# Optimization experiments

Measured on AMD Instinct MI355X. Metric: run time of the kernel, lower is better.

The kernel has to match this reference:

```python
import jax, jax.numpy as jnp
import numpy as np

D_MODEL = 1024
NUM_HEADS = 16
HEAD_DIM = D_MODEL // NUM_HEADS


def setup_inputs() -> dict:
    key = jax.random.key(0)
    k_x, k_wqkv, k_bqkv, k_wo, k_bo = jax.random.split(key, 5)
    s = 1.0 / np.sqrt(D_MODEL)
    return {
        "x": jax.random.normal(k_x, (4, 2048, D_MODEL), dtype=jnp.float32),
        "W_qkv": jax.random.uniform(k_wqkv, (D_MODEL, 3 * D_MODEL), jnp.float32, -s, s),
        "b_qkv": jax.random.uniform(k_bqkv, (3 * D_MODEL,), jnp.float32, -s, s),
        "W_out": jax.random.uniform(k_wo, (D_MODEL, D_MODEL), jnp.float32, -s, s),
        "b_out": jax.random.uniform(k_bo, (D_MODEL,), jnp.float32, -s, s),
    }


def reference(x, W_qkv, b_qkv, W_out, b_out):
    B, N, C = x.shape
    # fused QKV projection -> [B, N, 3, H, Dh]
    qkv = (x @ W_qkv + b_qkv).reshape(B, N, 3, NUM_HEADS, HEAD_DIM)
    q = jnp.transpose(qkv[:, :, 0], (0, 2, 1, 3))  # [B, H, N, Dh]
    k = jnp.transpose(qkv[:, :, 1], (0, 2, 1, 3))
    v = jnp.transpose(qkv[:, :, 2], (0, 2, 1, 3))
    scale = 1.0 / jnp.sqrt(jnp.asarray(HEAD_DIM, dtype=x.dtype))
    attn = jnp.einsum('bhqd,bhkd->bhqk', q, k) * scale  # [B, H, N, N]
    attn = jax.nn.softmax(attn, axis=-1)
    # dropout is identity in eval mode
    out = jnp.einsum('bhqk,bhkd->bhqd', attn, v)  # [B, H, N, Dh]
    out = jnp.transpose(out, (0, 2, 1, 3)).reshape(B, N, C)
    return out @ W_out + b_out
```

## Files before the change

kernel.cpp:

```cpp
#include <hip/hip_runtime.h>


typedef __bf16 bf16x8 __attribute__((ext_vector_type(8)));
typedef float f32x4 __attribute__((ext_vector_type(4)));

#define DEV __device__ __forceinline__

DEV unsigned short f2b(float x) {
  unsigned int u = __float_as_uint(x);
  u += 0x7fffu + ((u >> 16) & 1u);
  return (unsigned short)(u >> 16);
}

DEV unsigned int pk_bf16(float a, float b) {
  unsigned int ua = __float_as_uint(a) + 0x8000u;
  unsigned int ub = __float_as_uint(b) + 0x8000u;
  return __builtin_amdgcn_perm(ub, ua, 0x07060302u);
}

#if __has_builtin(__builtin_amdgcn_exp2f)
DEV float exp2_fast(float x) { return __builtin_amdgcn_exp2f(x); }
#else
DEV float exp2_fast(float x) { return exp2f(x); }
#endif

DEV void g2l16(const void* g, void* l) {
  __builtin_amdgcn_global_load_lds(
      (const __attribute__((address_space(1))) unsigned int*)(unsigned long long)g,
      (__attribute__((address_space(3))) unsigned int*)(unsigned int)(unsigned long long)l,
      16, 0, 0);
}

__global__ void cvt_x_kernel(const float* __restrict__ x,
                             unsigned short* __restrict__ xb) {
  int i = blockIdx.x * blockDim.x + threadIdx.x;
  float4 v = ((const float4*)x)[i];
  ushort4 o;
  o.x = f2b(v.x); o.y = f2b(v.y); o.z = f2b(v.z); o.w = f2b(v.w);
  ((ushort4*)xb)[i] = o;
}

__global__ void cvt_wt_kernel(const float* __restrict__ W,
                              unsigned short* __restrict__ Wt,
                              int K, int N) {
  __shared__ float tile[32][33];
  int n0 = blockIdx.x * 32, k0 = blockIdx.y * 32;
  int tx = threadIdx.x, ty = threadIdx.y;
#pragma unroll
  for (int i = 0; i < 32; i += 8)
    tile[ty + i][tx] = W[(size_t)(k0 + ty + i) * N + n0 + tx];
  __syncthreads();
#pragma unroll
  for (int i = 0; i < 32; i += 8)
    Wt[(size_t)(n0 + ty + i) * K + k0 + tx] = f2b(tile[tx][ty + i]);
}

#define QSCALE 0.18033688011112042f

template <int MODE>
__global__ __launch_bounds__(256, 2)
void gemm_bt_kernel(const unsigned short* __restrict__ A,
                    const unsigned short* __restrict__ Bt,
                    const float* __restrict__ bias,
                    unsigned short* __restrict__ qkout,
                    unsigned short* __restrict__ vtout,
                    float* __restrict__ fout) {
  constexpr int K = 1024;
  __shared__ unsigned short As[128 * 32];
  __shared__ unsigned short Bs[128 * 32];

  const int tid = threadIdx.x;
  const int lane = tid & 63;
  const int w = tid >> 6;
  const int wm = w & 1, wn = w >> 1;
  const int l15 = lane & 15, quad = lane >> 4;
  const int m0 = blockIdx.y * 128;
  const int n0 = blockIdx.x * 128;

  const unsigned short* Ag = A + (size_t)m0 * K;
  const unsigned short* Bg = Bt + (size_t)n0 * K;

  const int c0 = tid, c1 = tid + 256;
  const size_t ga0 = (size_t)(c0 >> 2) * K + (size_t)(c0 & 3) * 8;
  const size_t ga1 = (size_t)(c1 >> 2) * K + (size_t)(c1 & 3) * 8;
  unsigned short* la0 = &As[c0 * 8];
  unsigned short* la1 = &As[c1 * 8];
  unsigned short* lb0 = &Bs[c0 * 8];
  unsigned short* lb1 = &Bs[c1 * 8];

  f32x4 acc[4][4] = {};

  for (int kt = 0; kt < K; kt += 32) {
    g2l16(Ag + ga0 + kt, la0);
    g2l16(Ag + ga1 + kt, la1);
    g2l16(Bg + ga0 + kt, lb0);
    g2l16(Bg + ga1 + kt, lb1);
    __syncthreads();
    bf16x8 af[4], bfr[4];
#pragma unroll
    for (int i = 0; i < 4; ++i) {
      af[i]  = *(const bf16x8*)&As[(wm * 64 + i * 16 + l15) * 32 + quad * 8];
      bfr[i] = *(const bf16x8*)&Bs[(wn * 64 + i * 16 + l15) * 32 + quad * 8];
    }
#pragma unroll
    for (int mi = 0; mi < 4; ++mi)
#pragma unroll
      for (int ni = 0; ni < 4; ++ni)
        acc[mi][ni] = __builtin_amdgcn_mfma_f32_16x16x32_bf16(
            af[mi], bfr[ni], acc[mi][ni], 0, 0, 0);
    __syncthreads();
  }

  float bv[4];
#pragma unroll
  for (int ni = 0; ni < 4; ++ni)
    bv[ni] = bias[n0 + wn * 64 + ni * 16 + l15];

  if (MODE == 0) {
    const int sel = n0 >> 10;
    if (sel < 2) {
      const float scale = (sel == 0) ? QSCALE : 1.0f;
      const int csub = (n0 & 1023) + wn * 64;
#pragma unroll
      for (int mi = 0; mi < 4; ++mi) {
        int rb = m0 + wm * 64 + mi * 16 + quad * 4;
#pragma unroll
        for (int ni = 0; ni < 4; ++ni) {
          int c = csub + ni * 16 + l15;
#pragma unroll
          for (int r = 0; r < 4; ++r)
            qkout[(size_t)(rb + r) * 2048 + sel * 1024 + c] =
                f2b((acc[mi][ni][r] + bv[ni]) * scale);
        }
      }
    } else {
#pragma unroll
      for (int mi = 0; mi < 4; ++mi) {
        int rb = m0 + wm * 64 + mi * 16 + quad * 4;
        int bb = rb >> 11, n = rb & 2047;
#pragma unroll
        for (int ni = 0; ni < 4; ++ni) {
          int c = (n0 & 1023) + wn * 64 + ni * 16 + l15;
          int h = c >> 6, d = c & 63;
          ushort4 pk;
          pk.x = f2b(acc[mi][ni][0] + bv[ni]);
          pk.y = f2b(acc[mi][ni][1] + bv[ni]);
          pk.z = f2b(acc[mi][ni][2] + bv[ni]);
          pk.w = f2b(acc[mi][ni][3] + bv[ni]);
          *(ushort4*)&vtout[(((size_t)bb * 16 + h) * 64 + d) * 2048 + n] = pk;
        }
      }
    }
  } else {
#pragma unroll
    for (int mi = 0; mi < 4; ++mi) {
      int rb = m0 + wm * 64 + mi * 16 + quad * 4;
#pragma unroll
      for (int ni = 0; ni < 4; ++ni) {
        int c = n0 + wn * 64 + ni * 16 + l15;
#pragma unroll
        for (int r = 0; r < 4; ++r)
          fout[(size_t)(rb + r) * 1024 + c] = acc[mi][ni][r] + bv[ni];
      }
    }
  }
}

__global__ __launch_bounds__(256, 2)
void attn_kernel(const unsigned short* __restrict__ qk,
                 const unsigned short* __restrict__ vtg,
                 unsigned short* __restrict__ oat) {
  __shared__ unsigned short kt[64 * 72];
  __shared__ unsigned short vt[64 * 72];
  __shared__ unsigned short pt[256 * 72];

  const int tid = threadIdx.x;
  const int lane = tid & 63;
  const int w = tid >> 6;
  const int l15 = lane & 15, quad = lane >> 4;

  const int head = blockIdx.x * 8 + (blockIdx.y >> 3);
  const int qb = blockIdx.y & 7;
  const int b = head >> 4, h = head & 15;
  const int q0 = qb * 256;
  const size_t tokbase = (size_t)b * 2048;

  bf16x8 qf[4][2];
#pragma unroll
  for (int ni = 0; ni < 4; ++ni)
#pragma unroll
    for (int kc = 0; kc < 2; ++kc) {
      int q = q0 + w * 64 + ni * 16 + l15;
      qf[ni][kc] = *(const bf16x8*)(qk + (tokbase + q) * 2048 + h * 64 +
                                    kc * 32 + quad * 8);
    }

  f32x4 oacc[4][4] = {};
  float lsum[4] = {0.f, 0.f, 0.f, 0.f};

  const unsigned short* vhead = vtg + (size_t)head * 64 * 2048;
  const int srow = tid >> 3, spart = tid & 7;
  const int qrow = w * 64 + l15;

  uint4 kreg[2], vreg[2];
#pragma unroll
  for (int it = 0; it < 2; ++it) {
    int row = it * 32 + srow;
    kreg[it] = *(const uint4*)(qk + (tokbase + row) * 2048 + 1024 + h * 64 + spart * 8);
    vreg[it] = *(const uint4*)(vhead + (size_t)row * 2048 + spart * 8);
  }

  for (int kb = 0; kb < 2048; kb += 64) {
    __syncthreads();
#pragma unroll
    for (int it = 0; it < 2; ++it) {
      int row = it * 32 + srow;
      *(uint4*)&kt[row * 72 + spart * 8] = kreg[it];
      *(uint4*)&vt[row * 72 + spart * 8] = vreg[it];
    }
    __syncthreads();

    if (kb + 64 < 2048) {
#pragma unroll
      for (int it = 0; it < 2; ++it) {
        int row = it * 32 + srow;
        kreg[it] = *(const uint4*)(qk + (tokbase + kb + 64 + row) * 2048 + 1024 + h * 64 + spart * 8);
        vreg[it] = *(const uint4*)(vhead + (size_t)row * 2048 + kb + 64 + spart * 8);
      }
    }

    bf16x8 kf[4][2];
#pragma unroll
    for (int mi = 0; mi < 4; ++mi)
#pragma unroll
      for (int kc = 0; kc < 2; ++kc)
        kf[mi][kc] = *(const bf16x8*)&kt[(mi * 16 + l15) * 72 + kc * 32 + quad * 8];

#pragma unroll
    for (int nh = 0; nh < 2; ++nh) {
      f32x4 st[4][2];
#pragma unroll
      for (int mi = 0; mi < 4; ++mi)
#pragma unroll
        for (int nj = 0; nj < 2; ++nj) {
          f32x4 a = {0.f, 0.f, 0.f, 0.f};
          a = __builtin_amdgcn_mfma_f32_16x16x32_bf16(kf[mi][0], qf[nh * 2 + nj][0], a, 0, 0, 0);
          a = __builtin_amdgcn_mfma_f32_16x16x32_bf16(kf[mi][1], qf[nh * 2 + nj][1], a, 0, 0, 0);
          st[mi][nj] = a;
        }
#pragma unroll
      for (int nj = 0; nj < 2; ++nj) {
        int ni = nh * 2 + nj;
        float rs = 0.f;
#pragma unroll
        for (int mi = 0; mi < 4; ++mi) {
          float p0 = exp2_fast(st[mi][nj][0]);
          float p1 = exp2_fast(st[mi][nj][1]);
          float p2 = exp2_fast(st[mi][nj][2]);
          float p3 = exp2_fast(st[mi][nj][3]);
          rs += (p0 + p1) + (p2 + p3);
          uint2 pw;
          pw.x = pk_bf16(p0, p1);
          pw.y = pk_bf16(p2, p3);
          *(uint2*)&pt[(qrow + ni * 16) * 72 + mi * 16 + quad * 4] = pw;
        }
        lsum[ni] += rs;
      }
    }

    bf16x8 pf[4][2];
#pragma unroll
    for (int ni = 0; ni < 4; ++ni)
#pragma unroll
      for (int kc = 0; kc < 2; ++kc)
        pf[ni][kc] = *(const bf16x8*)&pt[(qrow + ni * 16) * 72 + kc * 32 + quad * 8];
#pragma unroll
    for (int df = 0; df < 4; ++df) {
#pragma unroll
      for (int kc = 0; kc < 2; ++kc) {
        bf16x8 vf = *(const bf16x8*)&vt[(df * 16 + l15) * 72 + kc * 32 + quad * 8];
#pragma unroll
        for (int ni = 0; ni < 4; ++ni)
          oacc[df][ni] = __builtin_amdgcn_mfma_f32_16x16x32_bf16(
              vf, pf[ni][kc], oacc[df][ni], 0, 0, 0);
      }
    }
  }

#pragma unroll
  for (int ni = 0; ni < 4; ++ni) {
    float s = lsum[ni];
    s += __shfl_xor(s, 16, 64);
    s += __shfl_xor(s, 32, 64);
    float inv = __builtin_amdgcn_rcpf(s);
    int q = q0 + w * 64 + ni * 16 + l15;
#pragma unroll
    for (int df = 0; df < 4; ++df) {
      uint2 pw;
      pw.x = pk_bf16(oacc[df][ni][0] * inv, oacc[df][ni][1] * inv);
      pw.y = pk_bf16(oacc[df][ni][2] * inv, oacc[df][ni][3] * inv);
      *(uint2*)&oat[(tokbase + q) * 1024 + h * 64 + df * 16 + quad * 4] = pw;
    }
  }
}

extern "C" void kernel_launch(void* const* d_in, const int* in_sizes, int n_in,
                              void* d_out, int out_size, void* d_ws, size_t ws_size,
                              hipStream_t stream) {
  const float* x    = (const float*)d_in[0];
  const float* Wqkv = (const float*)d_in[1];
  const float* bqkv = (const float*)d_in[2];
  const float* Wout = (const float*)d_in[3];
  const float* bout = (const float*)d_in[4];
  float* out = (float*)d_out;

  char* ws = (char*)d_ws;
  unsigned short* xb  = (unsigned short*)(ws + (size_t)0);
  unsigned short* wqt = (unsigned short*)(ws + ((size_t)16 << 20));
  unsigned short* wot = (unsigned short*)(ws + ((size_t)22 << 20));
  unsigned short* qkb = (unsigned short*)(ws + ((size_t)24 << 20));
  unsigned short* vtb = (unsigned short*)(ws + ((size_t)56 << 20));
  unsigned short* oat = (unsigned short*)(ws + ((size_t)72 << 20));

  cvt_x_kernel<<<8192, 256, 0, stream>>>(x, xb);
  cvt_wt_kernel<<<dim3(96, 32), dim3(32, 8), 0, stream>>>(Wqkv, wqt, 1024, 3072);
  cvt_wt_kernel<<<dim3(32, 32), dim3(32, 8), 0, stream>>>(Wout, wot, 1024, 1024);

  gemm_bt_kernel<0><<<dim3(24, 64), 256, 0, stream>>>(
      xb, wqt, bqkv, qkb, vtb, nullptr);

  attn_kernel<<<dim3(8, 64), 256, 0, stream>>>(qkb, vtb, oat);

  gemm_bt_kernel<1><<<dim3(8, 64), 256, 0, stream>>>(
      oat, wot, bout, nullptr, nullptr, out);
}
```

Measured before the change: 312.2 us.

## Pre-swizzle K and V into MFMA fragment layout and load directly to registers

The QKV projection epilogue now writes K and V in a per-head, per-64-key-tile fragment order that matches the MFMA operand layout, and Q goes to its own contiguous buffer. The attention kernel drops its shared-memory staging of K/V tiles and both block barriers per iteration. Each wave instead loads its fragments straight from global memory with coalesced 16-byte loads, double-buffered in registers. The cost is that every wave loads the full K/V tiles redundantly (four times per block, relying on cache), register pressure goes up, and the GEMM epilogue scatter for K is less coalesced.

```diff
diff --git a/kernel.cpp b/kernel.cpp
--- a/kernel.cpp
+++ b/kernel.cpp
@@ -62,8 +62,9 @@
 void gemm_bt_kernel(const unsigned short* __restrict__ A,
                     const unsigned short* __restrict__ Bt,
                     const float* __restrict__ bias,
-                    unsigned short* __restrict__ qkout,
-                    unsigned short* __restrict__ vtout,
+                    unsigned short* __restrict__ qout,
+                    unsigned short* __restrict__ kfrout,
+                    unsigned short* __restrict__ vfrout,
                     float* __restrict__ fout) {
   constexpr int K = 1024;
   __shared__ unsigned short As[128 * 32];
@@ -118,36 +119,57 @@
 
   if (MODE == 0) {
     const int sel = n0 >> 10;
-    if (sel < 2) {
-      const float scale = (sel == 0) ? QSCALE : 1.0f;
-      const int csub = (n0 & 1023) + wn * 64;
+    const int bbat = m0 >> 11;
+    const int ktb = ((m0 & 2047) >> 6) + wm;
+    if (sel == 0) {
 #pragma unroll
       for (int mi = 0; mi < 4; ++mi) {
         int rb = m0 + wm * 64 + mi * 16 + quad * 4;
 #pragma unroll
         for (int ni = 0; ni < 4; ++ni) {
-          int c = csub + ni * 16 + l15;
+          int c = (n0 & 1023) + wn * 64 + ni * 16 + l15;
 #pragma unroll
           for (int r = 0; r < 4; ++r)
-            qkout[(size_t)(rb + r) * 2048 + sel * 1024 + c] =
-                f2b((acc[mi][ni][r] + bv[ni]) * scale);
+            qout[(size_t)(rb + r) * 1024 + c] =
+                f2b((acc[mi][ni][r] + bv[ni]) * QSCALE);
+        }
+      }
+    } else if (sel == 1) {
+#pragma unroll
+      for (int ni = 0; ni < 4; ++ni) {
+        int c = (n0 & 1023) + wn * 64 + ni * 16 + l15;
+        int h = c >> 6, d = c & 63;
+        int kc = d >> 5, dq = (d >> 3) & 3, j = d & 7;
+        size_t fb = ((((size_t)(bbat * 16 + h) * 32 + ktb) * 8) + kc) * 512 +
+                    (size_t)(dq * 16) * 8 + j;
+#pragma unroll
+        for (int mi = 0; mi < 4; ++mi) {
+          size_t fm = fb + (size_t)mi * 1024;
+#pragma unroll
+          for (int r = 0; r < 4; ++r)
+            kfrout[fm + (quad * 4 + r) * 8] = f2b(acc[mi][ni][r] + bv[ni]);
         }
       }
     } else {
-#pragma unroll
-      for (int mi = 0; mi < 4; ++mi) {
-        int rb = m0 + wm * 64 + mi * 16 + quad * 4;
-        int bb = rb >> 11, n = rb & 2047;
-#pragma unroll
-        for (int ni = 0; ni < 4; ++ni) {
-          int c = (n0 & 1023) + wn * 64 + ni * 16 + l15;
-          int h = c >> 6, d = c & 63;
+      const int fqb = quad >> 1;
+      const int jj0 = (quad & 1) * 4;
+#pragma unroll
+      for (int ni = 0; ni < 4; ++ni) {
+        int c = (n0 & 1023) + wn * 64 + ni * 16 + l15;
+        int h = c >> 6, d = c & 63;
+        int df = d >> 4, fl15 = d & 15;
+#pragma unroll
+        for (int mi = 0; mi < 4; ++mi) {
+          int kc2 = mi >> 1;
+          int fquad = (mi & 1) * 2 + fqb;
+          size_t fb = ((((size_t)(bbat * 16 + h) * 32 + ktb) * 8) + df * 2 + kc2) * 512 +
+                      (size_t)(fquad * 16 + fl15) * 8 + jj0;
           ushort4 pk;
           pk.x = f2b(acc[mi][ni][0] + bv[ni]);
           pk.y = f2b(acc[mi][ni][1] + bv[ni]);
           pk.z = f2b(acc[mi][ni][2] + bv[ni]);
           pk.w = f2b(acc[mi][ni][3] + bv[ni]);
-          *(ushort4*)&vtout[(((size_t)bb * 16 + h) * 64 + d) * 2048 + n] = pk;
+          *(ushort4*)&vfrout[fb] = pk;
         }
       }
     }
@@ -167,11 +189,10 @@
 }
 
 __global__ __launch_bounds__(256, 2)
-void attn_kernel(const unsigned short* __restrict__ qk,
-                 const unsigned short* __restrict__ vtg,
+void attn_kernel(const unsigned short* __restrict__ qg,
+                 const unsigned short* __restrict__ kfr,
+                 const unsigned short* __restrict__ vfr,
                  unsigned short* __restrict__ oat) {
-  __shared__ unsigned short kt[64 * 72];
-  __shared__ unsigned short vt[64 * 72];
   __shared__ unsigned short pt[256 * 72];
 
   const int tid = threadIdx.x;
@@ -180,9 +201,8 @@
   const int l15 = lane & 15, quad = lane >> 4;
 
   const int head = blockIdx.x * 8 + (blockIdx.y >> 3);
-  const int qb = blockIdx.y & 7;
+  const int q0 = (blockIdx.y & 7) * 256;
   const int b = head >> 4, h = head & 15;
-  const int q0 = qb * 256;
   const size_t tokbase = (size_t)b * 2048;
 
   bf16x8 qf[4][2];
@@ -191,50 +211,35 @@
 #pragma unroll
     for (int kc = 0; kc < 2; ++kc) {
       int q = q0 + w * 64 + ni * 16 + l15;
-      qf[ni][kc] = *(const bf16x8*)(qk + (tokbase + q) * 2048 + h * 64 +
+      qf[ni][kc] = *(const bf16x8*)(qg + (tokbase + q) * 1024 + h * 64 +
                                     kc * 32 + quad * 8);
     }
 
   f32x4 oacc[4][4] = {};
   float lsum[4] = {0.f, 0.f, 0.f, 0.f};
 
-  const unsigned short* vhead = vtg + (size_t)head * 64 * 2048;
-  const int srow = tid >> 3, spart = tid & 7;
+  const bf16x8* kp = (const bf16x8*)kfr + (size_t)head * 32 * 512;
+  const bf16x8* vp = (const bf16x8*)vfr + (size_t)head * 32 * 512;
   const int qrow = w * 64 + l15;
 
-  uint4 kreg[2], vreg[2];
-#pragma unroll
-  for (int it = 0; it < 2; ++it) {
-    int row = it * 32 + srow;
-    kreg[it] = *(const uint4*)(qk + (tokbase + row) * 2048 + 1024 + h * 64 + spart * 8);
-    vreg[it] = *(const uint4*)(vhead + (size_t)row * 2048 + spart * 8);
-  }
-
-  for (int kb = 0; kb < 2048; kb += 64) {
-    __syncthreads();
-#pragma unroll
-    for (int it = 0; it < 2; ++it) {
-      int row = it * 32 + srow;
-      *(uint4*)&kt[row * 72 + spart * 8] = kreg[it];
-      *(uint4*)&vt[row * 72 + spart * 8] = vreg[it];
-    }
-    __syncthreads();
-
-    if (kb + 64 < 2048) {
-#pragma unroll
-      for (int it = 0; it < 2; ++it) {
-        int row = it * 32 + srow;
-        kreg[it] = *(const uint4*)(qk + (tokbase + kb + 64 + row) * 2048 + 1024 + h * 64 + spart * 8);
-        vreg[it] = *(const uint4*)(vhead + (size_t)row * 2048 + kb + 64 + spart * 8);
-      }
-    }
-
-    bf16x8 kf[4][2];
-#pragma unroll
-    for (int mi = 0; mi < 4; ++mi)
-#pragma unroll
-      for (int kc = 0; kc < 2; ++kc)
-        kf[mi][kc] = *(const bf16x8*)&kt[(mi * 16 + l15) * 72 + kc * 32 + quad * 8];
+  bf16x8 kfA[8], vfA[8];
+#pragma unroll
+  for (int f = 0; f < 8; ++f) {
+    kfA[f] = kp[f * 64 + lane];
+    vfA[f] = vp[f * 64 + lane];
+  }
+
+  for (int kt = 0; kt < 32; ++kt) {
+    bf16x8 kfB[8], vfB[8];
+    if (kt < 31) {
+      const bf16x8* kn = kp + (kt + 1) * 512;
+      const bf16x8* vn = vp + (kt + 1) * 512;
+#pragma unroll
+      for (int f = 0; f < 8; ++f) {
+        kfB[f] = kn[f * 64 + lane];
+        vfB[f] = vn[f * 64 + lane];
+      }
+    }
 
 #pragma unroll
     for (int nh = 0; nh < 2; ++nh) {
@@ -244,8 +249,8 @@
 #pragma unroll
         for (int nj = 0; nj < 2; ++nj) {
           f32x4 a = {0.f, 0.f, 0.f, 0.f};
-          a = __builtin_amdgcn_mfma_f32_16x16x32_bf16(kf[mi][0], qf[nh * 2 + nj][0], a, 0, 0, 0);
-          a = __builtin_amdgcn_mfma_f32_16x16x32_bf16(kf[mi][1], qf[nh * 2 + nj][1], a, 0, 0, 0);
+          a = __builtin_amdgcn_mfma_f32_16x16x32_bf16(kfA[mi * 2 + 0], qf[nh * 2 + nj][0], a, 0, 0, 0);
+          a = __builtin_amdgcn_mfma_f32_16x16x32_bf16(kfA[mi * 2 + 1], qf[nh * 2 + nj][1], a, 0, 0, 0);
           st[mi][nj] = a;
         }
 #pragma unroll
@@ -275,16 +280,16 @@
       for (int kc = 0; kc < 2; ++kc)
         pf[ni][kc] = *(const bf16x8*)&pt[(qrow + ni * 16) * 72 + kc * 32 + quad * 8];
 #pragma unroll
-    for (int df = 0; df < 4; ++df) {
-#pragma unroll
-      for (int kc = 0; kc < 2; ++kc) {
-        bf16x8 vf = *(const bf16x8*)&vt[(df * 16 + l15) * 72 + kc * 32 + quad * 8];
+    for (int df = 0; df < 4; ++df)
+#pragma unroll
+      for (int kc = 0; kc < 2; ++kc)
 #pragma unroll
         for (int ni = 0; ni < 4; ++ni)
           oacc[df][ni] = __builtin_amdgcn_mfma_f32_16x16x32_bf16(
-              vf, pf[ni][kc], oacc[df][ni], 0, 0, 0);
-      }
-    }
+              vfA[df * 2 + kc], pf[ni][kc], oacc[df][ni], 0, 0, 0);
+
+#pragma unroll
+    for (int f = 0; f < 8; ++f) { kfA[f] = kfB[f]; vfA[f] = vfB[f]; }
   }
 
 #pragma unroll
@@ -318,8 +323,9 @@
   unsigned short* xb  = (unsigned short*)(ws + (size_t)0);
   unsigned short* wqt = (unsigned short*)(ws + ((size_t)16 << 20));
   unsigned short* wot = (unsigned short*)(ws + ((size_t)22 << 20));
-  unsigned short* qkb = (unsigned short*)(ws + ((size_t)24 << 20));
-  unsigned short* vtb = (unsigned short*)(ws + ((size_t)56 << 20));
+  unsigned short* qbf = (unsigned short*)(ws + ((size_t)24 << 20));
+  unsigned short* kfr = (unsigned short*)(ws + ((size_t)40 << 20));
+  unsigned short* vfr = (unsigned short*)(ws + ((size_t)56 << 20));
   unsigned short* oat = (unsigned short*)(ws + ((size_t)72 << 20));
 
   cvt_x_kernel<<<8192, 256, 0, stream>>>(x, xb);
@@ -327,10 +333,10 @@
   cvt_wt_kernel<<<dim3(32, 32), dim3(32, 8), 0, stream>>>(Wout, wot, 1024, 1024);
 
   gemm_bt_kernel<0><<<dim3(24, 64), 256, 0, stream>>>(
-      xb, wqt, bqkv, qkb, vtb, nullptr);
-
-  attn_kernel<<<dim3(8, 64), 256, 0, stream>>>(qkb, vtb, oat);
+      xb, wqt, bqkv, qbf, kfr, vfr, nullptr);
+
+  attn_kernel<<<dim3(8, 64), 256, 0, stream>>>(qbf, kfr, vfr, oat);
 
   gemm_bt_kernel<1><<<dim3(8, 64), 256, 0, stream>>>(
-      oat, wot, bout, nullptr, nullptr, out);
-}
+      oat, wot, bout, nullptr, nullptr, nullptr, out);
+}
```

Result: faster. 275.7 us (-11.7%).
